# Kernel tuning notes

Measured on AMD Instinct MI355X. Metric: run time of the kernel, lower is better.

The kernel has to match this reference:

```python
import jax, jax.numpy as jnp
import numpy as np
from jax import lax

D = 64
ROWS, COLS = np.triu_indices(D)  # 2080 upper-triangular (row, col) pairs, row-major like the python loop
BN_S = 1.0 / np.sqrt(1.0 + 1e-5)  # inference BN with running_mean=0, running_var=1


def _bn_relu(x, g, b):
    # inference-mode BatchNorm2d (fresh running stats) followed by ReLU; x is NCHW
    return jax.nn.relu(x * (g * BN_S)[None, :, None, None] + b[None, :, None, None])


def _conv(x, w, stride, pad):
    return lax.conv_general_dilated(x, w, (stride, stride), [(pad, pad), (pad, pad)],
                                    dimension_numbers=('NCHW', 'OIHW', 'NCHW'))


def _block(x, g1, b1, w1, g2, b2, w2, stride, ws=None):
    xa = _bn_relu(x, g1, b1)
    y = _conv(xa, w1, stride, 1)
    y = _conv(_bn_relu(y, g2, b2), w2, 1, 1)
    sc = xa if ws is None else _conv(xa, ws, stride, 0)
    return y + sc


def _forward(x, y, conv_w, s1_g1, s1_b1, s1_w1, s1_g2, s1_b2, s1_w2,
             s2_g1, s2_b1, s2_w1, s2_g2, s2_b2, s2_w2, s2_ws,
             s3_g1, s3_b1, s3_w1, s3_g2, s3_b2, s3_w2, s3_ws,
             bn_g, bn_b, ct_w, ct_b):
    h = _conv(x, conv_w, 1, 1)                                   # (B,16,36,60)
    h = _block(h, s1_g1, s1_b1, s1_w1, s1_g2, s1_b2, s1_w2, 1)    # (B,16,36,60)
    h = _block(h, s2_g1, s2_b1, s2_w1, s2_g2, s2_b2, s2_w2, 2, s2_ws)  # (B,32,18,30)
    h = _block(h, s3_g1, s3_b1, s3_w1, s3_g2, s3_b2, s3_w2, 2, s3_ws)  # (B,64,9,15)
    h = _bn_relu(h, bn_g, bn_b)                                   # (B,64,9,15)
    xp = jnp.transpose(h, (0, 2, 3, 1))                           # (B,9,15,64) channels-last
    # triangular bilinear pooling: z[..., k] = x[..., row_k] * x[..., col_k]
    z = xp[..., ROWS] * xp[..., COLS]                             # (B,9,15,2080)
    # 1x1 conv d2 -> 64 ("condtoc") + channel gating
    A = jnp.einsum('bhwk,ok->bhwo', z, ct_w) + ct_b               # (B,9,15,64)
    G = jnp.mean(A, axis=(1, 2), keepdims=True)                   # (B,1,1,64) adaptive avg pool
    Dg = A * G + A
    out = xp * Dg + xp                                            # (B,9,15,64)
    return out


def setup_inputs() -> dict:
    key = jax.random.key(0)
    ks = iter(jax.random.split(key, 40))

    def rn(shape, scale=0.1):
        return jax.random.normal(next(ks), shape, dtype=jnp.float32) * scale

    def gm(shape):
        return jax.random.uniform(next(ks), shape, dtype=jnp.float32, minval=0.5, maxval=1.5)

    return {
        'x': rn((64, 3, 36, 60), 1.0), 'y': rn((64, 2), 1.0),
        'conv_w': rn((16, 3, 3, 3)),
        's1_g1': gm((16,)), 's1_b1': rn((16,)), 's1_w1': rn((16, 16, 3, 3)),
        's1_g2': gm((16,)), 's1_b2': rn((16,)), 's1_w2': rn((16, 16, 3, 3)),
        's2_g1': gm((16,)), 's2_b1': rn((16,)), 's2_w1': rn((32, 16, 3, 3)),
        's2_g2': gm((32,)), 's2_b2': rn((32,)), 's2_w2': rn((32, 32, 3, 3)),
        's2_ws': rn((32, 16, 1, 1)),
        's3_g1': gm((32,)), 's3_b1': rn((32,)), 's3_w1': rn((64, 32, 3, 3)),
        's3_g2': gm((64,)), 's3_b2': rn((64,)), 's3_w2': rn((64, 64, 3, 3)),
        's3_ws': rn((64, 32, 1, 1)),
        'bn_g': gm((64,)), 'bn_b': rn((64,)),
        'ct_w': rn((64, 2080), 0.02), 'ct_b': rn((64,), 0.02),
    }


def reference(x, y, conv_w, s1_g1, s1_b1, s1_w1, s1_g2, s1_b2, s1_w2,
              s2_g1, s2_b1, s2_w1, s2_g2, s2_b2, s2_w2, s2_ws,
              s3_g1, s3_b1, s3_w1, s3_g2, s3_b2, s3_w2, s3_ws,
              bn_g, bn_b, ct_w, ct_b):
    return _forward(x, y, conv_w, s1_g1, s1_b1, s1_w1, s1_g2, s1_b2, s1_w2,
                    s2_g1, s2_b1, s2_w1, s2_g2, s2_b2, s2_w2, s2_ws,
                    s3_g1, s3_b1, s3_w1, s3_g2, s3_b2, s3_w2, s3_ws,
                    bn_g, bn_b, ct_w, ct_b)
```

## Files before the change

kernel.cpp:

```cpp
#include <hip/hip_runtime.h>

#define BN_S 0.9999950000374997f

constexpr int BATCH = 64;

typedef __attribute__((ext_vector_type(8))) short bf16x8;
typedef __attribute__((ext_vector_type(4))) float f32x4;

__device__ __forceinline__ float bnrelu(float x, float gs, float bb) {
    return fmaxf(fmaf(x, gs, bb), 0.f);
}

__device__ __forceinline__ unsigned short f2bf(float f) {
    unsigned u = __builtin_bit_cast(unsigned, f);
    return (unsigned short)((u + 0x7FFFu + ((u >> 16) & 1u)) >> 16);
}
__device__ __forceinline__ float bf2f(unsigned short h) {
    unsigned u = ((unsigned)h) << 16;
    return __builtin_bit_cast(float, u);
}

template<int CIN, int CICH, int COUT, int CO_PER, int HIN, int WIN,
         int HOUT, int WOUT, int STRIDE, int ROWS, int P, int PARTS,
         bool PRE_BN, int SC, int CSC, int SSTR, int SCPARTS, bool WTL>
__device__ void convT_tile(float* smem, int band, int b, int zci,
    const float* __restrict__ in, size_t in_pstride,
    const float* __restrict__ w,
    const float* __restrict__ g, const float* __restrict__ bb,
    const float* __restrict__ xin, size_t xin_pstride,
    const float* __restrict__ g1v, const float* __restrict__ b1v,
    const float* __restrict__ wsc,
    float* __restrict__ out, size_t out_pstride)
{
    constexpr int IR = (STRIDE == 1) ? ROWS + 2 : 2 * ROWS + 1;
    constexpr int TW = (STRIDE == 1) ? WIN + 2 : WIN + 1;
    constexpr int AW = (P - 1) * STRIDE + 3;
    constexpr int PGW = WOUT / P;
    constexpr int NG = ROWS * PGW;
    constexpr int NITEMS = NG * (COUT / CO_PER);
    static_assert(NITEMS <= 256, "one item per thread");

    float* xs   = smem;
    float* wlds = xs + CICH * IR * TW;
    float* wscl = wlds + CICH * 9 * COUT;
    float* g1l  = wscl + ((SC == 2) ? CSC * COUT : 0);
    float* b1l  = g1l + (SC ? CSC : 0);

    const int ci0 = zci * CICH;
    const int r0 = band * ROWS;
    const int r0in = r0 * STRIDE - 1;
    const int tid = threadIdx.x;

    if constexpr (WTL) {
        const float* wsrc = w + (size_t)ci0 * 9 * COUT;
        for (int i = tid; i < CICH * 9 * COUT; i += 256) wlds[i] = wsrc[i];
    } else {
        for (int i = tid; i < CICH * 9 * COUT; i += 256) {
            int co = i % COUT; int rem = i / COUT; int tap = rem % 9; int ci = rem / 9;
            wlds[i] = w[((size_t)co * CIN + ci0 + ci) * 9 + tap];
        }
    }
    if constexpr (SC != 0) {
        if (tid < CSC) { g1l[tid] = g1v[tid] * BN_S; b1l[tid] = b1v[tid]; }
        if constexpr (SC == 2) {
            for (int i = tid; i < CSC * COUT; i += 256) {
                int co = i % COUT; int ci = i / COUT;
                wscl[i] = wsc[(size_t)co * CSC + ci];
            }
        }
    }
    for (int i = tid; i < CICH * IR * TW; i += 256) {
        int cc = i % TW; int rem = i / TW; int rr = rem % IR; int ci = rem / IR;
        int gr = r0in + rr; int gc = cc - 1;
        float v = 0.f;
        if (gr >= 0 && gr < HIN && gc >= 0 && gc < WIN) {
            size_t off = ((size_t)(b * CIN + ci0 + ci) * HIN + gr) * WIN + gc;
            v = in[off];
#pragma unroll
            for (int s = 1; s < PARTS; ++s) v += in[off + (size_t)s * in_pstride];
            if constexpr (PRE_BN) v = bnrelu(v, g[ci0 + ci] * BN_S, bb[ci0 + ci]);
        }
        xs[i] = v;
    }
    __syncthreads();

    if (tid < NITEMS) {
        const int it = tid;
        const int cog = it / NG; const int gi = it % NG;
        const int lr = gi / PGW; const int wc = (gi % PGW) * P;
        float acc[P][CO_PER];
#pragma unroll
        for (int j = 0; j < P; ++j)
#pragma unroll
            for (int co = 0; co < CO_PER; ++co) acc[j][co] = 0.f;

        for (int ci = 0; ci < CICH; ++ci) {
            const float* xb = xs + ((ci * IR) + lr * STRIDE) * TW + wc * STRIDE;
#pragma unroll
            for (int dh = 0; dh < 3; ++dh) {
                float aw[AW];
#pragma unroll
                for (int a = 0; a < AW; ++a) aw[a] = xb[dh * TW + a];
#pragma unroll
                for (int dw = 0; dw < 3; ++dw) {
                    const float* wp = wlds + (ci * 9 + dh * 3 + dw) * COUT + cog * CO_PER;
#pragma unroll
                    for (int c4 = 0; c4 < CO_PER; c4 += 4) {
                        float4 wv = *(const float4*)(wp + c4);
#pragma unroll
                        for (int j = 0; j < P; ++j) {
                            float a_ = aw[j * STRIDE + dw];
                            acc[j][c4 + 0] = fmaf(a_, wv.x, acc[j][c4 + 0]);
                            acc[j][c4 + 1] = fmaf(a_, wv.y, acc[j][c4 + 1]);
                            acc[j][c4 + 2] = fmaf(a_, wv.z, acc[j][c4 + 2]);
                            acc[j][c4 + 3] = fmaf(a_, wv.w, acc[j][c4 + 3]);
                        }
                    }
                }
            }
        }

        if constexpr (SC == 1) {
            if (zci == 0) {
#pragma unroll
                for (int co = 0; co < CO_PER; ++co) {
                    int c = cog * CO_PER + co;
#pragma unroll
                    for (int j = 0; j < P; ++j) {
                        size_t off = ((size_t)(b * CSC + c) * HOUT + (r0 + lr)) * WOUT + wc + j;
                        float v = xin[off];
#pragma unroll
                        for (int s = 1; s < SCPARTS; ++s) v += xin[off + s * xin_pstride];
                        acc[j][co] += bnrelu(v, g1l[c], b1l[c]);
                    }
                }
            }
        }
        if constexpr (SC == 2) {
            if (zci == 0) {
                const int hix = (r0 + lr) * SSTR;
                for (int ci = 0; ci < CSC; ++ci) {
                    float vv[P];
#pragma unroll
                    for (int j = 0; j < P; ++j) {
                        size_t off = ((size_t)(b * CSC + ci) * (HOUT * SSTR) + hix) * (WOUT * SSTR)
                                     + (wc + j) * SSTR;
                        float v = xin[off];
#pragma unroll
                        for (int s = 1; s < SCPARTS; ++s) v += xin[off + s * xin_pstride];
                        vv[j] = bnrelu(v, g1l[ci], b1l[ci]);
                    }
                    const float* wp = wscl + ci * COUT + cog * CO_PER;
#pragma unroll
                    for (int c4 = 0; c4 < CO_PER; c4 += 4) {
                        float4 wv = *(const float4*)(wp + c4);
#pragma unroll
                        for (int j = 0; j < P; ++j) {
                            acc[j][c4 + 0] = fmaf(vv[j], wv.x, acc[j][c4 + 0]);
                            acc[j][c4 + 1] = fmaf(vv[j], wv.y, acc[j][c4 + 1]);
                            acc[j][c4 + 2] = fmaf(vv[j], wv.z, acc[j][c4 + 2]);
                            acc[j][c4 + 3] = fmaf(vv[j], wv.w, acc[j][c4 + 3]);
                        }
                    }
                }
            }
        }

        float* op = out + (size_t)zci * out_pstride
                    + ((size_t)(b * COUT + cog * CO_PER) * HOUT + (r0 + lr)) * WOUT + wc;
#pragma unroll
        for (int co = 0; co < CO_PER; ++co)
#pragma unroll
            for (int j = 0; j < P; ++j)
                op[(size_t)co * HOUT * WOUT + j] = acc[j][co];
    }
}

template<int CIN, int CICH, int COUT, int CO_PER, int HIN, int WIN,
         int HOUT, int WOUT, int STRIDE, int ROWS, int P, int PARTS,
         bool PRE_BN, int SC, int CSC, int SSTR, int SCPARTS, bool WTL>
__global__ __launch_bounds__(256) void convT_k(
    const float* __restrict__ in, size_t in_pstride,
    const float* __restrict__ w,
    const float* __restrict__ g, const float* __restrict__ bb,
    const float* __restrict__ xin, size_t xin_pstride,
    const float* __restrict__ g1v, const float* __restrict__ b1v,
    const float* __restrict__ wsc,
    float* __restrict__ out, size_t out_pstride)
{
    constexpr int IR = (STRIDE == 1) ? ROWS + 2 : 2 * ROWS + 1;
    constexpr int TW = (STRIDE == 1) ? WIN + 2 : WIN + 1;
    constexpr int SM = CICH * IR * TW + CICH * 9 * COUT
                     + ((SC == 2) ? CSC * COUT : 0) + (SC ? 2 * CSC : 0);
    __shared__ __align__(16) float smem[SM];
    convT_tile<CIN, CICH, COUT, CO_PER, HIN, WIN, HOUT, WOUT, STRIDE, ROWS, P,
               PARTS, PRE_BN, SC, CSC, SSTR, SCPARTS, WTL>(
        smem, blockIdx.x, blockIdx.y, blockIdx.z,
        in, in_pstride, w, g, bb, xin, xin_pstride, g1v, b1v, wsc, out, out_pstride);
}

__global__ __launch_bounds__(256) void prep_k(
    const float* __restrict__ ctw, short* __restrict__ wf,
    const float* __restrict__ x, const float* __restrict__ conv_w,
    float* __restrict__ h0,
    const float* __restrict__ s1w1, const float* __restrict__ s1w2,
    const float* __restrict__ s2w1, const float* __restrict__ s2w2,
    const float* __restrict__ s3w1, const float* __restrict__ s3w2,
    float* __restrict__ wt)
{
    __shared__ __align__(16) float smem[3 * 8 * 62 + 3 * 9 * 16];
    int tl = blockIdx.x;
    if (tl < 768) {
        int id = tl * 256 + threadIdx.x;
        int j = id & 7; int lane = (id >> 3) & 63; int t4 = (id >> 9) & 3; int s = id >> 11;
        int c, ch;
        if (s < 32) { c = s; ch = 0; }
        else { c = 32 + ((s - 32) >> 1); ch = (s - 32) & 1; }
        int k = ch * 32 + ((lane >> 4) << 3) + j;
        int o = t4 * 16 + (lane & 15);
        float val = 0.f;
        if (k <= c) val = ctw[o * 2080 + (k * (129 - k)) / 2 + (c - k)];
        wf[id] = (short)f2bf(val);
    } else if (tl < 1152) {
        int tt = tl - 768;
        convT_tile<3, 3, 16, 8, 36, 60, 36, 60, 1, 6, 3, 1, false, 0, 1, 1, 1, false>(
            smem, tt % 6, tt / 6, 0, x, 0, conv_w, nullptr, nullptr,
            nullptr, 0, nullptr, nullptr, nullptr, h0, 0);
    } else {
        int id = (tl - 1152) * 256 + threadIdx.x;
        int base, CIN_, COUT_;
        const float* src;
        if (id < 2304)       { base = 0;     CIN_ = 16; COUT_ = 16; src = s1w1; }
        else if (id < 4608)  { base = 2304;  CIN_ = 16; COUT_ = 16; src = s1w2; }
        else if (id < 9216)  { base = 4608;  CIN_ = 16; COUT_ = 32; src = s2w1; }
        else if (id < 18432) { base = 9216;  CIN_ = 32; COUT_ = 32; src = s2w2; }
        else if (id < 36864) { base = 18432; CIN_ = 32; COUT_ = 64; src = s3w1; }
        else                 { base = 36864; CIN_ = 64; COUT_ = 64; src = s3w2; }
        int n = id - base;
        int co = n % COUT_; int tap = (n / COUT_) % 9; int ci = n / (9 * COUT_);
        wt[id] = src[((size_t)co * CIN_ + ci) * 9 + tap];
    }
}

__global__ __launch_bounds__(256) void red_k(
    const float* __restrict__ pb, const float* __restrict__ h2,
    const float* __restrict__ g1, const float* __restrict__ b1,
    const float* __restrict__ wsc, const float* __restrict__ bng,
    const float* __restrict__ bnb, float* __restrict__ xp)
{
    __shared__ float hsc[32][46];
    __shared__ float wscl[32][16];
    __shared__ float g1l[32], b1l[32];
    const int b = blockIdx.x, cq = blockIdx.y, pc = blockIdx.z;
    const int c0 = cq * 16;
    const int pbase = pc * 45;
    const int t = threadIdx.x;

    if (t < 32) { g1l[t] = g1[t] * BN_S; b1l[t] = b1[t]; }
    for (int i = t; i < 512; i += 256) {
        int ci = i & 31, cc = i >> 5;
        wscl[ci][cc] = wsc[(size_t)(c0 + cc) * 32 + ci];
    }
    __syncthreads();
    for (int i = t; i < 32 * 45; i += 256) {
        int ci = i / 45, pl = i % 45;
        int p = pbase + pl;
        int hp = p / 15, wp = p % 15;
        size_t off = ((size_t)(b * 32 + ci) * 18 + hp * 2) * 30 + wp * 2;
        float v = h2[off] + h2[off + 1105920] + h2[off + 2 * 1105920] + h2[off + 3 * 1105920];
        hsc[ci][pl] = bnrelu(v, g1l[ci], b1l[ci]);
    }
    __syncthreads();

    for (int e = t; e < 16 * 45; e += 256) {
        int cc = e / 45, pl = e % 45;
        int p = pbase + pl;
        int c = c0 + cc;
        size_t idx = ((size_t)(b * 64 + c)) * 135 + p;
        float y = 0.f;
#pragma unroll
        for (int q = 0; q < 8; ++q) y += pb[idx + (size_t)q * 552960];
#pragma unroll 8
        for (int ci = 0; ci < 32; ++ci) y = fmaf(hsc[ci][pl], wscl[ci][cc], y);
        xp[((size_t)b * 135 + p) * 64 + c] = bnrelu(y, bng[c] * BN_S, bnb[c]);
    }
}

template<int NCH>
__device__ void f2m_body(
    const unsigned short* xs, int q, const short* __restrict__ wf,
    const float* __restrict__ ctb, float* __restrict__ Abase, int p0, int t)
{
    float* A = Abase + (size_t)q * 552960;
    const int w = t >> 6, lane = t & 63;
    const int prow = w * 16;
    const int lrow = lane & 15, lk = lane >> 4;

    bf16x8 Af[NCH];
#pragma unroll
    for (int ch = 0; ch < NCH; ++ch) {
        int pix = prow + lrow;
        int g = ch * 4 + lk;
        Af[ch] = *(const bf16x8*)&xs[pix * 64 + ((g ^ (pix & 7)) * 8)];
    }

    f32x4 acc[4];
#pragma unroll
    for (int tt = 0; tt < 4; ++tt) acc[tt] = f32x4{0.f, 0.f, 0.f, 0.f};

    const int c0 = q * 16;
    bf16x8 BA[NCH][4], BB[NCH][4];

    auto loadB = [&](int c, bf16x8 (&B)[NCH][4]) {
        int slotb = (NCH == 1) ? c : (2 * c - 32);
#pragma unroll
        for (int ch = 0; ch < NCH; ++ch) {
            const short* wb = wf + (size_t)(slotb + ch) * 2048 + lane * 8;
#pragma unroll
            for (int tt = 0; tt < 4; ++tt)
                B[ch][tt] = *(const bf16x8*)(wb + tt * 512);
        }
    };
    auto compute = [&](int c, bf16x8 (&B)[NCH][4]) {
        f32x4 S[4];
#pragma unroll
        for (int tt = 0; tt < 4; ++tt) S[tt] = f32x4{0.f, 0.f, 0.f, 0.f};
#pragma unroll
        for (int ch = 0; ch < NCH; ++ch)
#pragma unroll
            for (int tt = 0; tt < 4; ++tt)
                S[tt] = __builtin_amdgcn_mfma_f32_16x16x32_bf16(Af[ch], B[ch][tt], S[tt], 0, 0, 0);
#pragma unroll
        for (int j = 0; j < 4; ++j) {
            int pix = prow + lk * 4 + j;
            float sv = bf2f(xs[pix * 64 + (((c >> 3) ^ (pix & 7)) * 8) + (c & 7)]);
#pragma unroll
            for (int tt = 0; tt < 4; ++tt)
                acc[tt][j] += sv * S[tt][j];
        }
    };

    loadB(c0, BA);
#pragma unroll 1
    for (int ci = 0; ci < 16; ci += 2) {
        loadB(c0 + ci + 1, BB);
        compute(c0 + ci, BA);
        if (ci < 14) loadB(c0 + ci + 2, BA);
        compute(c0 + ci + 1, BB);
    }

#pragma unroll
    for (int j = 0; j < 4; ++j) {
        int gpix = p0 + prow + lk * 4 + j;
#pragma unroll
        for (int tt = 0; tt < 4; ++tt) {
            int o = tt * 16 + lrow;
            float vv = acc[tt][j];
            if (q == 0) vv += ctb[o];
            A[(size_t)gpix * 64 + o] = vv;
        }
    }
}

__global__ __launch_bounds__(256) void f2m_k(
    const float* __restrict__ xp, const short* __restrict__ wf,
    const float* __restrict__ ctb, float* __restrict__ Abase)
{
    __shared__ unsigned short xs[64 * 64];
    const int t = threadIdx.x;
    const int p0 = blockIdx.x * 64;
    const int q = blockIdx.y;

    {
        int pr = t >> 2, seg = t & 3;
        const float4* src = (const float4*)(xp + (size_t)(p0 + pr) * 64 + seg * 16);
        float v[16];
#pragma unroll
        for (int i = 0; i < 4; ++i) {
            float4 x4 = src[i];
            v[i*4+0] = x4.x; v[i*4+1] = x4.y; v[i*4+2] = x4.z; v[i*4+3] = x4.w;
        }
#pragma unroll
        for (int gi = 0; gi < 2; ++gi) {
            unsigned w0 = f2bf(v[gi*8+0]) | ((unsigned)f2bf(v[gi*8+1]) << 16);
            unsigned w1 = f2bf(v[gi*8+2]) | ((unsigned)f2bf(v[gi*8+3]) << 16);
            unsigned w2 = f2bf(v[gi*8+4]) | ((unsigned)f2bf(v[gi*8+5]) << 16);
            unsigned w3 = f2bf(v[gi*8+6]) | ((unsigned)f2bf(v[gi*8+7]) << 16);
            int grp = seg * 2 + gi;
            int sg = grp ^ (pr & 7);
            *(uint4*)&xs[pr * 64 + sg * 8] = make_uint4(w0, w1, w2, w3);
        }
    }
    __syncthreads();

    if (q < 2) f2m_body<1>(xs, q, wf, ctb, Abase, p0, t);
    else       f2m_body<2>(xs, q, wf, ctb, Abase, p0, t);
}

__global__ void f3a_k(const float* __restrict__ A, float* __restrict__ G)
{
    int b = blockIdx.x; int t = threadIdx.x;
    int o = t & 63; int grp = t >> 6;
    float s = 0.f;
    for (int p = grp; p < 135; p += 4) {
        size_t off = ((size_t)b * 135 + p) * 64 + o;
        s += A[off] + A[off + 552960] + A[off + 2 * 552960] + A[off + 3 * 552960];
    }
    __shared__ float red[4][64];
    red[grp][o] = s;
    __syncthreads();
    if (t < 64) G[b * 64 + t] = (red[0][t] + red[1][t] + red[2][t] + red[3][t]) * (1.0f / 135.0f);
}

__global__ void f3b_k(const float* __restrict__ xp, const float* __restrict__ A,
                      const float* __restrict__ G, float* __restrict__ out)
{
    int idx = blockIdx.x * 256 + threadIdx.x;
    if (idx >= BATCH * 135 * 64) return;
    int o = idx & 63; int b = idx / (135 * 64);
    float a = A[idx] + A[idx + 552960] + A[idx + 2 * 552960] + A[idx + 3 * 552960];
    float g = G[b * 64 + o];
    float x = xp[idx];
    out[idx] = fmaf(x, a * (g + 1.f), x);
}

extern "C" void kernel_launch(void* const* d_in, const int* in_sizes, int n_in,
                              void* d_out, int out_size, void* d_ws, size_t ws_size,
                              hipStream_t stream)
{
    const float* x      = (const float*)d_in[0];
    const float* conv_w = (const float*)d_in[2];
    const float* s1_g1  = (const float*)d_in[3];
    const float* s1_b1  = (const float*)d_in[4];
    const float* s1_w1  = (const float*)d_in[5];
    const float* s1_g2  = (const float*)d_in[6];
    const float* s1_b2  = (const float*)d_in[7];
    const float* s1_w2  = (const float*)d_in[8];
    const float* s2_g1  = (const float*)d_in[9];
    const float* s2_b1  = (const float*)d_in[10];
    const float* s2_w1  = (const float*)d_in[11];
    const float* s2_g2  = (const float*)d_in[12];
    const float* s2_b2  = (const float*)d_in[13];
    const float* s2_w2  = (const float*)d_in[14];
    const float* s2_ws  = (const float*)d_in[15];
    const float* s3_g1  = (const float*)d_in[16];
    const float* s3_b1  = (const float*)d_in[17];
    const float* s3_w1  = (const float*)d_in[18];
    const float* s3_g2  = (const float*)d_in[19];
    const float* s3_b2  = (const float*)d_in[20];
    const float* s3_w2  = (const float*)d_in[21];
    const float* s3_ws  = (const float*)d_in[22];
    const float* bn_g   = (const float*)d_in[23];
    const float* bn_b   = (const float*)d_in[24];
    const float* ct_w   = (const float*)d_in[25];
    const float* ct_b   = (const float*)d_in[26];
    float* out = (float*)d_out;

    float* ws = (float*)d_ws;
    float* h0      = ws + 0;
    float* p_b1c1  = ws + 2211840;
    float* p_h1    = ws + 6635520;
    float* p_b2c1  = ws + 11059200;
    float* p_b2c2  = ws + 13271040;
    float* p_b3c1  = ws + 17694720;
    float* p_b3c2  = ws + 19906560;
    float* xp      = ws + 24330240;
    float* A       = ws + 24883200;
    short* wfrag   = (short*)(ws + 27095040);
    float* wt      = ws + 27193344;
    float* G       = ws + 27267072;

    dim3 blk(256);

    prep_k<<<1440, blk, 0, stream>>>(ct_w, wfrag, x, conv_w, h0,
                                     s1_w1, s1_w2, s2_w1, s2_w2, s3_w1, s3_w2, wt);

    convT_k<16, 8, 16, 4, 36, 60, 36, 60, 1, 4, 5, 1, true, 0, 1, 1, 1, true>
        <<<dim3(9, 64, 2), blk, 0, stream>>>(
        h0, 0, wt + 0, s1_g1, s1_b1, nullptr, 0, nullptr, nullptr, nullptr,
        p_b1c1, 2211840);
    convT_k<16, 8, 16, 4, 36, 60, 36, 60, 1, 4, 5, 2, true, 1, 16, 1, 1, true>
        <<<dim3(9, 64, 2), blk, 0, stream>>>(
        p_b1c1, 2211840, wt + 2304, s1_g2, s1_b2, h0, 0, s1_g1, s1_b1, nullptr,
        p_h1, 2211840);
    convT_k<16, 8, 32, 4, 36, 60, 18, 30, 2, 3, 3, 2, true, 0, 1, 1, 1, true>
        <<<dim3(6, 64, 2), blk, 0, stream>>>(
        p_h1, 2211840, wt + 4608, s2_g1, s2_b1, nullptr, 0, nullptr, nullptr, nullptr,
        p_b2c1, 1105920);
    convT_k<32, 8, 32, 4, 18, 30, 18, 30, 1, 3, 3, 2, true, 2, 16, 2, 2, true>
        <<<dim3(6, 64, 4), blk, 0, stream>>>(
        p_b2c1, 1105920, wt + 9216, s2_g2, s2_b2, p_h1, 2211840, s2_g1, s2_b1, s2_ws,
        p_b2c2, 1105920);
    convT_k<32, 8, 64, 4, 18, 30, 9, 15, 2, 3, 3, 4, true, 0, 1, 1, 1, true>
        <<<dim3(3, 64, 4), blk, 0, stream>>>(
        p_b2c2, 1105920, wt + 18432, s3_g1, s3_b1, nullptr, 0, nullptr, nullptr, nullptr,
        p_b3c1, 552960);
    convT_k<64, 8, 64, 4, 9, 15, 9, 15, 1, 3, 3, 4, true, 0, 1, 1, 1, true>
        <<<dim3(3, 64, 8), blk, 0, stream>>>(
        p_b3c1, 552960, wt + 36864, s3_g2, s3_b2, nullptr, 0, nullptr, nullptr, nullptr,
        p_b3c2, 552960);
    red_k<<<dim3(64, 4, 3), blk, 0, stream>>>(p_b3c2, p_b2c2,
                                              s3_g1, s3_b1, s3_ws, bn_g, bn_b, xp);
    f2m_k<<<dim3(135, 4), blk, 0, stream>>>(xp, wfrag, ct_b, A);
    f3a_k<<<64, blk, 0, stream>>>(A, G);
    f3b_k<<<2160, blk, 0, stream>>>(xp, A, G, out);
}
```

Before: 166.6 us.

## Reduce split-K partials in conv stages and fuse gating reduction with output

Raises the input-channel chunk sizes in several conv launches, which cuts the number of split-K partial buffers that later stages must sum. Block-1 convs now write a single output instead of two partials, and the final 64-channel conv writes four partials instead of eight. The reduction kernel is adjusted to match, and the workspace layout shrinks. The two final kernels (mean pooling and gating) are merged into one: each block recomputes its batch's channel means in shared memory, then applies gating to one fifth of that batch. This trades redundant mean recomputation and less grid parallelism in the convs for fewer launches and less partial-sum traffic.

```diff
diff --git a/kernel.cpp b/kernel.cpp
--- a/kernel.cpp
+++ b/kernel.cpp
@@ -279,7 +279,7 @@
         size_t idx = ((size_t)(b * 64 + c)) * 135 + p;
         float y = 0.f;
 #pragma unroll
-        for (int q = 0; q < 8; ++q) y += pb[idx + (size_t)q * 552960];
+        for (int q = 0; q < 4; ++q) y += pb[idx + (size_t)q * 552960];
 #pragma unroll 8
         for (int ci = 0; ci < 32; ++ci) y = fmaf(hsc[ci][pl], wscl[ci][cc], y);
         xp[((size_t)b * 135 + p) * 64 + c] = bnrelu(y, bng[c] * BN_S, bnb[c]);
@@ -397,31 +397,35 @@
     else       f2m_body<2>(xs, q, wf, ctb, Abase, p0, t);
 }
 
-__global__ void f3a_k(const float* __restrict__ A, float* __restrict__ G)
-{
-    int b = blockIdx.x; int t = threadIdx.x;
-    int o = t & 63; int grp = t >> 6;
+__global__ __launch_bounds__(256) void f3_k(
+    const float* __restrict__ xp, const float* __restrict__ A,
+    float* __restrict__ out)
+{
+    __shared__ float red[256];
+    __shared__ float gG[64];
+    const int b = blockIdx.x, cz = blockIdx.y;
+    const int t = threadIdx.x;
+    const int o = t & 63, grp = t >> 6;
+
     float s = 0.f;
     for (int p = grp; p < 135; p += 4) {
         size_t off = ((size_t)b * 135 + p) * 64 + o;
         s += A[off] + A[off + 552960] + A[off + 2 * 552960] + A[off + 3 * 552960];
     }
-    __shared__ float red[4][64];
-    red[grp][o] = s;
+    red[grp * 64 + o] = s;
     __syncthreads();
-    if (t < 64) G[b * 64 + t] = (red[0][t] + red[1][t] + red[2][t] + red[3][t]) * (1.0f / 135.0f);
-}
-
-__global__ void f3b_k(const float* __restrict__ xp, const float* __restrict__ A,
-                      const float* __restrict__ G, float* __restrict__ out)
-{
-    int idx = blockIdx.x * 256 + threadIdx.x;
-    if (idx >= BATCH * 135 * 64) return;
-    int o = idx & 63; int b = idx / (135 * 64);
-    float a = A[idx] + A[idx + 552960] + A[idx + 2 * 552960] + A[idx + 3 * 552960];
-    float g = G[b * 64 + o];
-    float x = xp[idx];
-    out[idx] = fmaf(x, a * (g + 1.f), x);
+    if (t < 64)
+        gG[t] = (red[t] + red[64 + t] + red[128 + t] + red[192 + t]) * (1.0f / 135.0f);
+    __syncthreads();
+
+    const size_t base = (size_t)b * 8640;
+    for (int e = cz * 1728 + t; e < (cz + 1) * 1728; e += 256) {
+        size_t idx = base + e;
+        int oo = e & 63;
+        float a = A[idx] + A[idx + 552960] + A[idx + 2 * 552960] + A[idx + 3 * 552960];
+        float x = xp[idx];
+        out[idx] = fmaf(x, a * (gG[oo] + 1.f), x);
+    }
 }
 
 extern "C" void kernel_launch(void* const* d_in, const int* in_sizes, int n_in,
@@ -458,50 +462,48 @@
 
     float* ws = (float*)d_ws;
     float* h0      = ws + 0;
-    float* p_b1c1  = ws + 2211840;
-    float* p_h1    = ws + 6635520;
-    float* p_b2c1  = ws + 11059200;
-    float* p_b2c2  = ws + 13271040;
-    float* p_b3c1  = ws + 17694720;
-    float* p_b3c2  = ws + 19906560;
-    float* xp      = ws + 24330240;
-    float* A       = ws + 24883200;
-    short* wfrag   = (short*)(ws + 27095040);
-    float* wt      = ws + 27193344;
-    float* G       = ws + 27267072;
+    float* y1      = ws + 2211840;
+    float* h1      = ws + 4423680;
+    float* p_b2c1  = ws + 6635520;
+    float* p_b2c2  = ws + 8847360;
+    float* p_b3c1  = ws + 13271040;
+    float* p_b3c2  = ws + 15482880;
+    float* xp      = ws + 17694720;
+    float* A       = ws + 18247680;
+    short* wfrag   = (short*)(ws + 20459520);
+    float* wt      = ws + 20557824;
 
     dim3 blk(256);
 
     prep_k<<<1440, blk, 0, stream>>>(ct_w, wfrag, x, conv_w, h0,
                                      s1_w1, s1_w2, s2_w1, s2_w2, s3_w1, s3_w2, wt);
 
-    convT_k<16, 8, 16, 4, 36, 60, 36, 60, 1, 4, 5, 1, true, 0, 1, 1, 1, true>
-        <<<dim3(9, 64, 2), blk, 0, stream>>>(
+    convT_k<16, 16, 16, 4, 36, 60, 36, 60, 1, 4, 5, 1, true, 0, 1, 1, 1, true>
+        <<<dim3(9, 64, 1), blk, 0, stream>>>(
         h0, 0, wt + 0, s1_g1, s1_b1, nullptr, 0, nullptr, nullptr, nullptr,
-        p_b1c1, 2211840);
-    convT_k<16, 8, 16, 4, 36, 60, 36, 60, 1, 4, 5, 2, true, 1, 16, 1, 1, true>
-        <<<dim3(9, 64, 2), blk, 0, stream>>>(
-        p_b1c1, 2211840, wt + 2304, s1_g2, s1_b2, h0, 0, s1_g1, s1_b1, nullptr,
-        p_h1, 2211840);
-    convT_k<16, 8, 32, 4, 36, 60, 18, 30, 2, 3, 3, 2, true, 0, 1, 1, 1, true>
+        y1, 0);
+    convT_k<16, 16, 16, 4, 36, 60, 36, 60, 1, 4, 5, 1, true, 1, 16, 1, 1, true>
+        <<<dim3(9, 64, 1), blk, 0, stream>>>(
+        y1, 0, wt + 2304, s1_g2, s1_b2, h0, 0, s1_g1, s1_b1, nullptr,
+        h1, 0);
+    convT_k<16, 8, 32, 4, 36, 60, 18, 30, 2, 3, 3, 1, true, 0, 1, 1, 1, true>
         <<<dim3(6, 64, 2), blk, 0, stream>>>(
-        p_h1, 2211840, wt + 4608, s2_g1, s2_b1, nullptr, 0, nullptr, nullptr, nullptr,
+        h1, 0, wt + 4608, s2_g1, s2_b1, nullptr, 0, nullptr, nullptr, nullptr,
         p_b2c1, 1105920);
-    convT_k<32, 8, 32, 4, 18, 30, 18, 30, 1, 3, 3, 2, true, 2, 16, 2, 2, true>
+    convT_k<32, 8, 32, 4, 18, 30, 18, 30, 1, 3, 3, 2, true, 2, 16, 2, 1, true>
         <<<dim3(6, 64, 4), blk, 0, stream>>>(
-        p_b2c1, 1105920, wt + 9216, s2_g2, s2_b2, p_h1, 2211840, s2_g1, s2_b1, s2_ws,
+        p_b2c1, 1105920, wt + 9216, s2_g2, s2_b2, h1, 0, s2_g1, s2_b1, s2_ws,
         p_b2c2, 1105920);
     convT_k<32, 8, 64, 4, 18, 30, 9, 15, 2, 3, 3, 4, true, 0, 1, 1, 1, true>
         <<<dim3(3, 64, 4), blk, 0, stream>>>(
         p_b2c2, 1105920, wt + 18432, s3_g1, s3_b1, nullptr, 0, nullptr, nullptr, nullptr,
         p_b3c1, 552960);
-    convT_k<64, 8, 64, 4, 9, 15, 9, 15, 1, 3, 3, 4, true, 0, 1, 1, 1, true>
-        <<<dim3(3, 64, 8), blk, 0, stream>>>(
+    convT_k<64, 16, 64, 4, 9, 15, 9, 15, 1, 3, 3, 4, true, 0, 1, 1, 1, true>
+        <<<dim3(3, 64, 4), blk, 0, stream>>>(
         p_b3c1, 552960, wt + 36864, s3_g2, s3_b2, nullptr, 0, nullptr, nullptr, nullptr,
         p_b3c2, 552960);
     red_k<<<dim3(64, 4, 3), blk, 0, stream>>>(p_b3c2, p_b2c2,
                                               s3_g1, s3_b1, s3_ws, bn_g, bn_b, xp);
     f2m_k<<<dim3(135, 4), blk, 0, stream>>>(xp, wfrag, ct_b, A);
-    f3a_k<<<64, blk, 0, stream>>>(A, G);
-    f3b_k<<<2160, blk, 0, stream>>>(xp, A, G, out);
-}
+    f3_k<<<dim3(64, 5), blk, 0, stream>>>(xp, A, out);
+}
```

After: 179.2 us. 7.6% more time.
